# Kernel tuning notes

Hardware: AMD Instinct MI355X
Metric: run time of the kernel (lower is better)

## Reference

```python
import jax, jax.numpy as jnp
import numpy as np

WS = (4, 4, 4)      # window size (d, h, w)
SS = (2, 2, 2)      # shift size
HEADS = 4
EPS = 1e-6          # flax LayerNorm default epsilon


def _rel_pos_index(ws):
    # replicates the source exactly (np.meshgrid default 'xy' indexing)
    coords = np.stack(np.meshgrid(np.arange(ws[0]), np.arange(ws[1]), np.arange(ws[2])))
    cf = coords.reshape(3, -1)
    rc = (cf[:, :, None] - cf[:, None, :]).transpose(1, 2, 0).astype(np.int64)
    rc[:, :, 0] += ws[0] - 1
    rc[:, :, 1] += ws[1] - 1
    rc[:, :, 2] += ws[2] - 1
    rc[:, :, 0] *= (2 * ws[1] - 1) * (2 * ws[2] - 1)
    rc[:, :, 1] *= 2 * ws[2] - 1
    return rc.sum(-1)  # (n, n)


def _compute_mask(dp, hp, wp, ws, ss):
    # standard shifted-window attention mask: (nw, n, n) with 0 / -100
    img = np.zeros((1, dp, hp, wp, 1), np.float32)
    cnt = 0
    sls = lambda w, s: (slice(0, -w), slice(-w, -s), slice(-s, None))
    for d in sls(ws[0], ss[0]):
        for h in sls(ws[1], ss[1]):
            for w in sls(ws[2], ss[2]):
                img[:, d, h, w, :] = cnt
                cnt += 1
    mw = img.reshape(1, dp // ws[0], ws[0], hp // ws[1], ws[1], wp // ws[2], ws[2], 1)
    mw = mw.transpose(0, 1, 3, 5, 2, 4, 6, 7).reshape(-1, ws[0] * ws[1] * ws[2])
    am = mw[:, None, :] - mw[:, :, None]
    return np.where(am != 0, np.float32(-100.0), np.float32(0.0))


def window_partition(x, ws):
    b, d, h, w, c = x.shape
    x = x.reshape(b, d // ws[0], ws[0], h // ws[1], ws[1], w // ws[2], ws[2], c)
    return x.transpose(0, 1, 3, 5, 2, 4, 6, 7).reshape(-1, ws[0] * ws[1] * ws[2], c)


def window_reverse(windows, ws, dims):
    b, d, h, w = dims
    x = windows.reshape(b, d // ws[0], h // ws[1], w // ws[2], ws[0], ws[1], ws[2], -1)
    return x.transpose(0, 1, 4, 2, 5, 3, 6, 7).reshape(b, d, h, w, -1)


def layernorm(x, scale, bias):
    m = x.mean(-1, keepdims=True)
    v = x.var(-1, keepdims=True)
    return (x - m) * jax.lax.rsqrt(v + EPS) * scale + bias


def setup_inputs() -> dict:
    key = jax.random.key(0)
    ks = jax.random.split(key, 8)
    B, D, H, W, C = 2, 32, 64, 64, 128
    HID = 4 * C
    p = 0.02
    return {
        "x": jax.random.normal(ks[0], (B, D, H, W, C), jnp.float32),
        "mask": jnp.asarray(_compute_mask(D, H, W, WS, SS)),
        "norm1_scale": jnp.ones((C,), jnp.float32),
        "norm1_bias": jnp.zeros((C,), jnp.float32),
        "qkv_w": jax.random.normal(ks[1], (C, 3 * C), jnp.float32) * p,
        "rel_bias_table": jax.random.normal(ks[2], ((2 * WS[0] - 1) * (2 * WS[1] - 1) * (2 * WS[2] - 1), HEADS), jnp.float32) * p,
        "proj_w": jax.random.normal(ks[3], (C, C), jnp.float32) * p,
        "proj_b": jnp.zeros((C,), jnp.float32),
        "norm2_scale": jnp.ones((C,), jnp.float32),
        "norm2_bias": jnp.zeros((C,), jnp.float32),
        "mlp_w1": jax.random.normal(ks[4], (C, HID), jnp.float32) * p,
        "mlp_b1": jnp.zeros((HID,), jnp.float32),
        "mlp_w2": jax.random.normal(ks[5], (HID, C), jnp.float32) * p,
        "mlp_b2": jnp.zeros((C,), jnp.float32),
    }


def reference(x, mask, norm1_scale, norm1_bias, qkv_w, rel_bias_table, proj_w, proj_b,
              norm2_scale, norm2_bias, mlp_w1, mlp_b1, mlp_w2, mlp_b2):
    b, d, h, w, c = x.shape
    hd = c // HEADS
    scale = hd ** -0.5
    n = WS[0] * WS[1] * WS[2]

    shortcut = x
    xn = layernorm(x, norm1_scale, norm1_bias)
    # cyclic shift + window partition
    shifted = jnp.roll(xn, shift=(-SS[0], -SS[1], -SS[2]), axis=(1, 2, 3))
    xw = window_partition(shifted, WS)                      # (b*nw, n, c)
    bw = xw.shape[0]

    qkv = (xw @ qkv_w).reshape(bw, n, 3, HEADS, hd).transpose(2, 0, 3, 1, 4)
    q, k, v = qkv[0] * scale, qkv[1], qkv[2]                # (bw, heads, n, hd)
    attn = jnp.einsum('bhqd,bhkd->bhqk', q, k)              # (bw, heads, n, n)

    idx = _rel_pos_index(WS)
    bias = rel_bias_table[idx.reshape(-1)].reshape(n, n, HEADS).transpose(2, 0, 1)
    attn = attn + bias[None]

    nw = mask.shape[0]
    attn = attn.reshape(bw // nw, nw, HEADS, n, n) + mask[None, :, None]
    attn = jax.nn.softmax(attn.reshape(bw, HEADS, n, n), axis=-1)

    out = jnp.einsum('bhqk,bhkd->bhqd', attn, v)
    out = jnp.swapaxes(out, 1, 2).reshape(bw, n, c)
    out = out @ proj_w + proj_b

    attn_out = window_reverse(out, WS, (b, d, h, w))
    attn_out = jnp.roll(attn_out, shift=SS, axis=(1, 2, 3))

    x = shortcut + attn_out
    xn2 = layernorm(x, norm2_scale, norm2_bias)
    m = jax.nn.gelu(xn2 @ mlp_w1 + mlp_b1) @ mlp_w2 + mlp_b2
    return x + m
```

## Files before the change

kernel.cpp:

```cpp
#include <hip/hip_runtime.h>

typedef __bf16 bf16x8 __attribute__((ext_vector_type(8)));
typedef float f32x4 __attribute__((ext_vector_type(4)));
typedef unsigned short u16x4 __attribute__((ext_vector_type(4)));
typedef unsigned short u16x8 __attribute__((ext_vector_type(8)));

#define MFMA16(a,b,c) __builtin_amdgcn_mfma_f32_16x16x32_bf16((a),(b),(c),0,0,0)

__device__ __forceinline__ unsigned short f2bf(float f){
  return __builtin_bit_cast(unsigned short, static_cast<__bf16>(f));
}
__device__ __forceinline__ float bf2f(unsigned short h){
  unsigned u = ((unsigned)h)<<16;
  return __builtin_bit_cast(float, u);
}
__device__ __forceinline__ bf16x8 g_frag(const unsigned short* __restrict__ wf, int fragIdx, int lane){
  return __builtin_bit_cast(bf16x8, *reinterpret_cast<const u16x8*>(wf + (size_t)(fragIdx*64 + lane)*8));
}
__device__ __forceinline__ bf16x8 lds_frag(const unsigned short* base, int fragIdx, int lane){
  return __builtin_bit_cast(bf16x8, *reinterpret_cast<const u16x8*>(base + (fragIdx*64 + lane)*8));
}
__device__ __forceinline__ bf16x8 bc(u16x8 v){ return __builtin_bit_cast(bf16x8, v); }

__global__ void pack_w_kernel(const float* __restrict__ src, unsigned short* __restrict__ dst,
                              int MT, int KP, int M){
  int tid = blockIdx.x*256 + threadIdx.x;
  if (tid >= MT*KP*64) return;
  int lane = tid & 63;
  int t2 = tid >> 6;
  int kp = t2 % KP;
  int m = 16*(t2 / KP) + (lane & 15);
  int g = lane >> 4;
  u16x8 v;
#pragma unroll
  for (int j = 0; j < 8; ++j) {
    int k = 4*g + (j&3) + 16*(j>>2) + 32*kp;
    v[j] = f2bf(src[k*M + m]);
  }
  *reinterpret_cast<u16x8*>(&dst[(size_t)tid*8]) = v;
}

__global__ void prep_bias_kernel(const float* __restrict__ table, float* __restrict__ bias2){
  int o = blockIdx.x*256 + threadIdx.x;
  if (o >= 4*4*4*64*4) return;
  int r2 = o&3, lane = (o>>2)&63, nt = (o>>8)&3, mt = (o>>10)&3, h = o>>12;
  int g = lane>>4, l15 = lane&15;
  int key = 16*mt + 4*g + r2, q = 16*nt + l15;
  int da = ((q>>2)&3) - ((key>>2)&3) + 3;
  int ha = (q>>4)     - (key>>4)     + 3;
  int wa = (q&3)      - (key&3)      + 3;
  bias2[o] = table[((da*7+ha)*7+wa)*4 + h];
}

__global__ __launch_bounds__(256, 2)
void swin_block_kernel(const float* __restrict__ x,
                       const float* __restrict__ n1s, const float* __restrict__ n1b,
                       const unsigned short* __restrict__ wqk,
                       const unsigned short* __restrict__ wvb,
                       const float* __restrict__ bias2,
                       const unsigned short* __restrict__ wproj,
                       const float* __restrict__ projb,
                       const float* __restrict__ n2s, const float* __restrict__ n2b,
                       const unsigned short* __restrict__ w1f, const float* __restrict__ b1,
                       const unsigned short* __restrict__ w2f, const float* __restrict__ b2,
                       float* __restrict__ out)
{
  __shared__ __align__(16) unsigned short ldsA[16*64*8];
  __shared__ __align__(16) unsigned short ldsH[16*64*8];
  __shared__ int rid_s[64];

  const int tid  = threadIdx.x;
  const int lane = tid & 63;
  const int w    = tid >> 6;
  const int g    = lane >> 4;
  const int l15  = lane & 15;

  const int wb = blockIdx.x;
  const int b  = wb >> 11;
  const int r0 = wb & 2047;
  const int bd = r0 >> 8, bh = (r0 >> 4) & 15, bwi = r0 & 15;

  const int t = tid >> 2, qtr = tid & 3;
  const int wd = t >> 4, wh = (t >> 2) & 3, ww = t & 3;
  const int dco = (bd*4 + wd + 2) & 31;
  const int hco = (bh*4 + wh + 2) & 63;
  const int wco = (bwi*4 + ww + 2) & 63;
  const long tokl = ((long)((b*32 + dco)*64 + hco))*64 + wco;
  const float* xrow = x + tokl*128 + qtr*32;
  const int tileT = t >> 4, l15t = t & 15;

  u16x8 rsd[4];
  {
    float xr[32];
    float s = 0.f, sq = 0.f;
#pragma unroll
    for (int i = 0; i < 8; ++i) {
      float4 v = reinterpret_cast<const float4*>(xrow)[i];
      xr[4*i+0]=v.x; xr[4*i+1]=v.y; xr[4*i+2]=v.z; xr[4*i+3]=v.w;
      s  += v.x + v.y + v.z + v.w;
      sq += v.x*v.x + v.y*v.y + v.z*v.z + v.w*v.w;
    }
    s  += __shfl_xor(s, 1);  s  += __shfl_xor(s, 2);
    sq += __shfl_xor(sq, 1); sq += __shfl_xor(sq, 2);
    const float mean = s * 0.0078125f;
    const float rs   = rsqrtf(sq * 0.0078125f - mean*mean + 1e-6f);
#pragma unroll
    for (int i = 0; i < 8; ++i) {
      u16x4 o4;
#pragma unroll
      for (int j2 = 0; j2 < 4; ++j2) {
        int c = qtr*32 + 4*i + j2;
        o4[j2] = f2bf((xr[4*i+j2]-mean)*rs*n1s[c] + n1b[c]);
        rsd[i>>1][4*(i&1)+j2] = f2bf(xr[4*i+j2]);
      }
      *reinterpret_cast<u16x4*>(&ldsA[((tileT*4+qtr)*64 + l15t + 16*(i&3))*8 + 4*(i>>2)]) = o4;
    }
  }
  if (tid < 64) {
    int twd = tid >> 4, twh = (tid >> 2) & 3, tww = tid & 3;
    int rd = (bd == 7)  ? (twd < 2 ? 1 : 2) : 0;
    int rh = (bh == 15) ? (twh < 2 ? 1 : 2) : 0;
    int rw = (bwi == 15)? (tww < 2 ? 1 : 2) : 0;
    rid_s[tid] = rd*9 + rh*3 + rw;
  }
  __syncthreads();

  u16x8 Qf[4], Kf[4], Vf[2][2];
  {
    f32x4 acc[2][4];
#pragma unroll
    for (int mi=0;mi<2;++mi)
#pragma unroll
      for (int nt=0;nt<4;++nt){ f32x4 z={0.f,0.f,0.f,0.f}; acc[mi][nt]=z; }
#pragma unroll
    for (int kp=0;kp<4;++kp){
      bf16x8 bx[4];
#pragma unroll
      for (int nt=0;nt<4;++nt) bx[nt] = lds_frag(ldsA, nt*4+kp, lane);
#pragma unroll
      for (int mi=0;mi<2;++mi){
        bf16x8 a = g_frag(wqk, (2*w+mi)*4+kp, lane);
#pragma unroll
        for (int nt=0;nt<4;++nt) acc[mi][nt] = MFMA16(a, bx[nt], acc[mi][nt]);
      }
    }
#pragma unroll
    for (int nt=0;nt<4;++nt){
      u16x8 v;
#pragma unroll
      for (int j=0;j<8;++j) v[j] = f2bf(acc[j>>2][nt][j&3]*0.17677669529663687f);
      Qf[nt]=v;
    }
#pragma unroll
    for (int mi=0;mi<2;++mi)
#pragma unroll
      for (int nt=0;nt<4;++nt){ f32x4 z={0.f,0.f,0.f,0.f}; acc[mi][nt]=z; }
#pragma unroll
    for (int kp=0;kp<4;++kp){
      bf16x8 bx[4];
#pragma unroll
      for (int nt=0;nt<4;++nt) bx[nt] = lds_frag(ldsA, nt*4+kp, lane);
#pragma unroll
      for (int mi=0;mi<2;++mi){
        bf16x8 a = g_frag(wqk, (8+2*w+mi)*4+kp, lane);
#pragma unroll
        for (int nt=0;nt<4;++nt) acc[mi][nt] = MFMA16(a, bx[nt], acc[mi][nt]);
      }
    }
#pragma unroll
    for (int nt=0;nt<4;++nt){
      u16x8 v;
#pragma unroll
      for (int j=0;j<8;++j) v[j] = f2bf(acc[j>>2][nt][j&3]);
      Kf[nt]=v;
    }
    f32x4 vacc[4][2];
#pragma unroll
    for (int mt=0;mt<4;++mt)
#pragma unroll
      for (int c2=0;c2<2;++c2){ f32x4 z={0.f,0.f,0.f,0.f}; vacc[mt][c2]=z; }
#pragma unroll
    for (int kp=0;kp<4;++kp){
      bf16x8 ax[4];
#pragma unroll
      for (int mt=0;mt<4;++mt) ax[mt] = lds_frag(ldsA, mt*4+kp, lane);
#pragma unroll
      for (int c2=0;c2<2;++c2){
        bf16x8 bv = g_frag(wvb, (2*w+c2)*4+kp, lane);
#pragma unroll
        for (int mt=0;mt<4;++mt) vacc[mt][c2] = MFMA16(ax[mt], bv, vacc[mt][c2]);
      }
    }
#pragma unroll
    for (int c2=0;c2<2;++c2)
#pragma unroll
      for (int kpk=0;kpk<2;++kpk){
        u16x8 v;
#pragma unroll
        for (int j=0;j<8;++j) v[j] = f2bf(vacc[(j>>2)+2*kpk][c2][j&3]);
        Vf[c2][kpk]=v;
      }
  }
  __syncthreads();

  {
#pragma unroll
    for (int nt=0;nt<4;++nt){
      f32x4 sacc[4];
#pragma unroll
      for (int mt=0;mt<4;++mt){
        f32x4 z = {0.f,0.f,0.f,0.f};
        sacc[mt] = MFMA16(bc(Kf[mt]), bc(Qf[nt]), z);
      }
      const int ridq = rid_s[16*nt + l15];
#pragma unroll
      for (int mt=0;mt<4;++mt){
        int4 rk = *reinterpret_cast<const int4*>(&rid_s[16*mt + 4*g]);
        float4 bv = reinterpret_cast<const float4*>(bias2)[((w*4+mt)*4+nt)*64 + lane];
        sacc[mt][0] += bv.x + (rk.x != ridq ? -100.f : 0.f);
        sacc[mt][1] += bv.y + (rk.y != ridq ? -100.f : 0.f);
        sacc[mt][2] += bv.z + (rk.z != ridq ? -100.f : 0.f);
        sacc[mt][3] += bv.w + (rk.w != ridq ? -100.f : 0.f);
      }
      float mx = -1e30f;
#pragma unroll
      for (int mt=0;mt<4;++mt)
#pragma unroll
        for (int r2=0;r2<4;++r2) mx = fmaxf(mx, sacc[mt][r2]);
      mx = fmaxf(mx, __shfl_xor(mx, 16));
      mx = fmaxf(mx, __shfl_xor(mx, 32));
      float sum = 0.f;
#pragma unroll
      for (int mt=0;mt<4;++mt)
#pragma unroll
        for (int r2=0;r2<4;++r2){
          float p = __expf(sacc[mt][r2] - mx);
          sacc[mt][r2] = p; sum += p;
        }
      sum += __shfl_xor(sum, 16);
      sum += __shfl_xor(sum, 32);
      const float inv = 1.f / sum;
      u16x8 Pf0, Pf1;
#pragma unroll
      for (int j=0;j<8;++j){
        Pf0[j] = f2bf(sacc[(j>>2)  ][j&3]*inv);
        Pf1[j] = f2bf(sacc[(j>>2)+2][j&3]*inv);
      }
      f32x4 oa[2];
#pragma unroll
      for (int c2=0;c2<2;++c2){
        f32x4 z = {0.f,0.f,0.f,0.f};
        z = MFMA16(bc(Vf[c2][0]), bc(Pf0), z);
        oa[c2] = MFMA16(bc(Vf[c2][1]), bc(Pf1), z);
      }
      u16x8 v;
#pragma unroll
      for (int j=0;j<8;++j) v[j] = f2bf(oa[j>>2][j&3]);
      *reinterpret_cast<u16x8*>(&ldsA[((nt*4+w)*64+lane)*8]) = v;
    }
  }
  __syncthreads();

  {
    f32x4 pacc[2][4];
#pragma unroll
    for (int mi=0;mi<2;++mi)
#pragma unroll
      for (int nt=0;nt<4;++nt){ f32x4 z={0.f,0.f,0.f,0.f}; pacc[mi][nt]=z; }
#pragma unroll
    for (int kp=0;kp<4;++kp){
      bf16x8 bo[4];
#pragma unroll
      for (int nt=0;nt<4;++nt) bo[nt] = lds_frag(ldsA, nt*4+kp, lane);
#pragma unroll
      for (int mi=0;mi<2;++mi){
        bf16x8 a = g_frag(wproj, (2*w+mi)*4+kp, lane);
#pragma unroll
        for (int nt=0;nt<4;++nt) pacc[mi][nt] = MFMA16(a, bo[nt], pacc[mi][nt]);
      }
    }
#pragma unroll
    for (int mi=0;mi<2;++mi)
#pragma unroll
      for (int r2=0;r2<4;++r2){
        const float pb = projb[16*(2*w+mi) + 4*g + r2];
#pragma unroll
        for (int nt=0;nt<4;++nt) pacc[mi][nt][r2] += pb;
      }
    __syncthreads();
#pragma unroll
    for (int nt=0;nt<4;++nt){
      u16x8 v;
#pragma unroll
      for (int j=0;j<8;++j) v[j] = f2bf(pacc[j>>2][nt][j&3]);
      *reinterpret_cast<u16x8*>(&ldsA[((nt*4+w)*64+lane)*8]) = v;
    }
  }
  __syncthreads();

  {
    float xv[32];
    float s2 = 0.f, sq2 = 0.f;
#pragma unroll
    for (int i = 0; i < 8; ++i) {
      u16x4 sg = *reinterpret_cast<const u16x4*>(&ldsA[((tileT*4+qtr)*64 + l15t + 16*(i&3))*8 + 4*(i>>2)]);
#pragma unroll
      for (int j2 = 0; j2 < 4; ++j2) {
        float v2 = bf2f(rsd[i>>1][4*(i&1)+j2]) + bf2f(sg[j2]);
        xv[4*i+j2] = v2;
        s2 += v2; sq2 += v2*v2;
      }
    }
    s2  += __shfl_xor(s2, 1);  s2  += __shfl_xor(s2, 2);
    sq2 += __shfl_xor(sq2, 1); sq2 += __shfl_xor(sq2, 2);
    const float mean2 = s2*0.0078125f;
    const float rs2 = rsqrtf(sq2*0.0078125f - mean2*mean2 + 1e-6f);
#pragma unroll
    for (int i = 0; i < 8; ++i) {
      u16x4 o4;
#pragma unroll
      for (int j2 = 0; j2 < 4; ++j2) {
        int c = qtr*32 + 4*i + j2;
        o4[j2] = f2bf((xv[4*i+j2]-mean2)*rs2*n2s[c] + n2b[c]);
        rsd[i>>1][4*(i&1)+j2] = f2bf(xv[4*i+j2]);
      }
      *reinterpret_cast<u16x4*>(&ldsA[((tileT*4+qtr)*64 + l15t + 16*(i&3))*8 + 4*(i>>2)]) = o4;
    }
  }
  __syncthreads();

  {
    f32x4 macc[2][4];
#pragma unroll
    for (int mi=0;mi<2;++mi)
#pragma unroll
      for (int nt=0;nt<4;++nt){ f32x4 z={0.f,0.f,0.f,0.f}; macc[mi][nt]=z; }
#pragma unroll
    for (int cc=0;cc<4;++cc){
      f32x4 hacc[2][4];
#pragma unroll
      for (int mi=0;mi<2;++mi)
#pragma unroll
        for (int nt=0;nt<4;++nt){ f32x4 z={0.f,0.f,0.f,0.f}; hacc[mi][nt]=z; }
#pragma unroll
      for (int kp=0;kp<4;++kp){
        bf16x8 bn[4];
#pragma unroll
        for (int nt=0;nt<4;++nt) bn[nt] = lds_frag(ldsA, nt*4+kp, lane);
#pragma unroll
        for (int mi=0;mi<2;++mi){
          bf16x8 a = g_frag(w1f, (cc*8+2*w+mi)*4+kp, lane);
#pragma unroll
          for (int nt=0;nt<4;++nt) hacc[mi][nt] = MFMA16(a, bn[nt], hacc[mi][nt]);
        }
      }
#pragma unroll
      for (int nt=0;nt<4;++nt){
        u16x8 hv;
#pragma unroll
        for (int j=0;j<8;++j){
          const int mi = j>>2, r2 = j&3;
          const int hch = cc*128 + 32*w + 16*mi + 4*g + r2;
          float v2 = hacc[mi][nt][r2] + b1[hch];
          float gg = 0.7978845608028654f*(v2 + 0.044715f*v2*v2*v2);
          float ge = v2 / (1.f + __expf(-2.f*gg));
          hv[j] = f2bf(ge);
        }
        *reinterpret_cast<u16x8*>(&ldsH[((nt*4+w)*64+lane)*8]) = hv;
      }
      __syncthreads();
#pragma unroll
      for (int kph=0;kph<4;++kph){
        bf16x8 bhf[4];
#pragma unroll
        for (int nt=0;nt<4;++nt) bhf[nt] = lds_frag(ldsH, nt*4+kph, lane);
#pragma unroll
        for (int mi=0;mi<2;++mi){
          bf16x8 a2 = g_frag(w2f, (2*w+mi)*16 + cc*4 + kph, lane);
#pragma unroll
          for (int nt=0;nt<4;++nt) macc[mi][nt] = MFMA16(a2, bhf[nt], macc[mi][nt]);
        }
      }
      __syncthreads();
    }
#pragma unroll
    for (int nt=0;nt<4;++nt){
      u16x8 v;
#pragma unroll
      for (int j=0;j<8;++j){
        const int mi = j>>2, r2 = j&3;
        v[j] = f2bf(macc[mi][nt][r2] + b2[16*(2*w+mi) + 4*g + r2]);
      }
      *reinterpret_cast<u16x8*>(&ldsA[((nt*4+w)*64+lane)*8]) = v;
    }
  }
  __syncthreads();

  {
    float* orow = out + tokl*128 + qtr*32;
#pragma unroll
    for (int i = 0; i < 8; ++i) {
      u16x4 mv = *reinterpret_cast<const u16x4*>(&ldsA[((tileT*4+qtr)*64 + l15t + 16*(i&3))*8 + 4*(i>>2)]);
      float4 v;
      v.x = bf2f(rsd[i>>1][4*(i&1)+0]) + bf2f(mv[0]);
      v.y = bf2f(rsd[i>>1][4*(i&1)+1]) + bf2f(mv[1]);
      v.z = bf2f(rsd[i>>1][4*(i&1)+2]) + bf2f(mv[2]);
      v.w = bf2f(rsd[i>>1][4*(i&1)+3]) + bf2f(mv[3]);
      reinterpret_cast<float4*>(orow)[i] = v;
    }
  }
}

extern "C" void kernel_launch(void* const* d_in, const int* in_sizes, int n_in,
                              void* d_out, int out_size, void* d_ws, size_t ws_size,
                              hipStream_t stream) {
  (void)in_sizes; (void)n_in; (void)out_size; (void)ws_size;
  const float* x    = (const float*)d_in[0];
  const float* n1s  = (const float*)d_in[2];
  const float* n1b  = (const float*)d_in[3];
  const float* qkvw = (const float*)d_in[4];
  const float* tbl  = (const float*)d_in[5];
  const float* pw   = (const float*)d_in[6];
  const float* pb   = (const float*)d_in[7];
  const float* n2s  = (const float*)d_in[8];
  const float* n2b  = (const float*)d_in[9];
  const float* w1   = (const float*)d_in[10];
  const float* b1   = (const float*)d_in[11];
  const float* w2   = (const float*)d_in[12];
  const float* b2   = (const float*)d_in[13];
  float* out = (float*)d_out;

  unsigned short* wqk_f   = (unsigned short*)d_ws;
  unsigned short* wvb_f   = wqk_f   + 16*4*64*8;
  unsigned short* wproj_f = wvb_f   + 8*4*64*8;
  unsigned short* w1_f    = wproj_f + 8*4*64*8;
  unsigned short* w2_f    = w1_f    + 32*4*64*8;
  float*          bias2   = (float*)(w2_f + 8*16*64*8);

  pack_w_kernel<<<16, 256, 0, stream>>>(qkvw,       wqk_f,  16, 4, 384);
  pack_w_kernel<<< 8, 256, 0, stream>>>(qkvw + 256, wvb_f,   8, 4, 384);
  pack_w_kernel<<< 8, 256, 0, stream>>>(pw,   wproj_f, 8, 4, 128);
  pack_w_kernel<<<32, 256, 0, stream>>>(w1,   w1_f,   32, 4, 512);
  pack_w_kernel<<<32, 256, 0, stream>>>(w2,   w2_f,    8,16, 128);
  prep_bias_kernel<<<64, 256, 0, stream>>>(tbl, bias2);

  swin_block_kernel<<<4096, 256, 0, stream>>>(x, n1s, n1b, wqk_f, wvb_f, bias2, wproj_f, pb,
                                              n2s, n2b, w1_f, b1, w2_f, b2, out);
}
```

Baseline: 496.2 us.

## Restructure proj/MLP to per-wave token tiles, fuse QKV loops and prep kernels

The projection and MLP stages are reorganized so each wave owns one 16-token tile and computes all output channels. The MLP hidden activations then stay in registers and feed the second GEMM directly, which removes the per-chunk LDS round trip and the block barriers. The Q, K and V projections share a single loop over LDS fragments. The shift mask is skipped for interior windows, and the six prep launches are merged into one kernel. In exchange, each wave now loads the full weight matrices from global memory, and the kernel carries more accumulator registers.

```diff
diff --git a/kernel.cpp b/kernel.cpp
--- a/kernel.cpp
+++ b/kernel.cpp
@@ -22,9 +22,9 @@
 }
 __device__ __forceinline__ bf16x8 bc(u16x8 v){ return __builtin_bit_cast(bf16x8, v); }
 
-__global__ void pack_w_kernel(const float* __restrict__ src, unsigned short* __restrict__ dst,
-                              int MT, int KP, int M){
-  int tid = blockIdx.x*256 + threadIdx.x;
+__device__ __forceinline__ void pack_body(const float* __restrict__ src, unsigned short* __restrict__ dst,
+                                          int blk, int MT, int KP, int M){
+  int tid = blk*256 + threadIdx.x;
   if (tid >= MT*KP*64) return;
   int lane = tid & 63;
   int t2 = tid >> 6;
@@ -40,16 +40,27 @@
   *reinterpret_cast<u16x8*>(&dst[(size_t)tid*8]) = v;
 }
 
-__global__ void prep_bias_kernel(const float* __restrict__ table, float* __restrict__ bias2){
-  int o = blockIdx.x*256 + threadIdx.x;
-  if (o >= 4*4*4*64*4) return;
+__global__ void prep_kernel(const float* __restrict__ qkvw, const float* __restrict__ pw,
+                            const float* __restrict__ w1, const float* __restrict__ w2,
+                            const float* __restrict__ tbl,
+                            unsigned short* __restrict__ wqk_f, unsigned short* __restrict__ wvb_f,
+                            unsigned short* __restrict__ wproj_f,
+                            unsigned short* __restrict__ w1_f, unsigned short* __restrict__ w2_f,
+                            float* __restrict__ bias2){
+  const int bb = blockIdx.x;
+  if (bb < 16)      { pack_body(qkvw,       wqk_f,   bb,      16, 4, 384); return; }
+  else if (bb < 24) { pack_body(qkvw + 256, wvb_f,   bb-16,    8, 4, 384); return; }
+  else if (bb < 32) { pack_body(pw,         wproj_f, bb-24,    8, 4, 128); return; }
+  else if (bb < 64) { pack_body(w1,         w1_f,    bb-32,   32, 4, 512); return; }
+  else if (bb < 96) { pack_body(w2,         w2_f,    bb-64,    8,16, 128); return; }
+  const int o = (bb-96)*256 + threadIdx.x;
   int r2 = o&3, lane = (o>>2)&63, nt = (o>>8)&3, mt = (o>>10)&3, h = o>>12;
   int g = lane>>4, l15 = lane&15;
   int key = 16*mt + 4*g + r2, q = 16*nt + l15;
   int da = ((q>>2)&3) - ((key>>2)&3) + 3;
   int ha = (q>>4)     - (key>>4)     + 3;
   int wa = (q&3)      - (key&3)      + 3;
-  bias2[o] = table[((da*7+ha)*7+wa)*4 + h];
+  bias2[o] = tbl[((da*7+ha)*7+wa)*4 + h];
 }
 
 __global__ __launch_bounds__(256, 2)
@@ -79,6 +90,7 @@
   const int b  = wb >> 11;
   const int r0 = wb & 2047;
   const int bd = r0 >> 8, bh = (r0 >> 4) & 15, bwi = r0 & 15;
+  const bool edge = (bd==7) || (bh==15) || (bwi==15);
 
   const int t = tid >> 2, qtr = tid & 3;
   const int wd = t >> 4, wh = (t >> 2) & 3, ww = t & 3;
@@ -116,7 +128,7 @@
       *reinterpret_cast<u16x4*>(&ldsA[((tileT*4+qtr)*64 + l15t + 16*(i&3))*8 + 4*(i>>2)]) = o4;
     }
   }
-  if (tid < 64) {
+  if (edge && tid < 64) {
     int twd = tid >> 4, twh = (tid >> 2) & 3, tww = tid & 3;
     int rd = (bd == 7)  ? (twd < 2 ? 1 : 2) : 0;
     int rh = (bh == 15) ? (twh < 2 ? 1 : 2) : 0;
@@ -127,69 +139,44 @@
 
   u16x8 Qf[4], Kf[4], Vf[2][2];
   {
-    f32x4 acc[2][4];
-#pragma unroll
-    for (int mi=0;mi<2;++mi)
-#pragma unroll
-      for (int nt=0;nt<4;++nt){ f32x4 z={0.f,0.f,0.f,0.f}; acc[mi][nt]=z; }
+    f32x4 qacc[2][4], kacc[2][4], vacc[4][2];
+#pragma unroll
+    for (int a2=0;a2<2;++a2)
+#pragma unroll
+      for (int b4=0;b4<4;++b4){ f32x4 z={0.f,0.f,0.f,0.f}; qacc[a2][b4]=z; kacc[a2][b4]=z; vacc[b4][a2]=z; }
 #pragma unroll
     for (int kp=0;kp<4;++kp){
-      bf16x8 bx[4];
-#pragma unroll
-      for (int nt=0;nt<4;++nt) bx[nt] = lds_frag(ldsA, nt*4+kp, lane);
+      bf16x8 fx[4];
+#pragma unroll
+      for (int nt=0;nt<4;++nt) fx[nt] = lds_frag(ldsA, nt*4+kp, lane);
 #pragma unroll
       for (int mi=0;mi<2;++mi){
-        bf16x8 a = g_frag(wqk, (2*w+mi)*4+kp, lane);
-#pragma unroll
-        for (int nt=0;nt<4;++nt) acc[mi][nt] = MFMA16(a, bx[nt], acc[mi][nt]);
-      }
-    }
-#pragma unroll
-    for (int nt=0;nt<4;++nt){
-      u16x8 v;
-#pragma unroll
-      for (int j=0;j<8;++j) v[j] = f2bf(acc[j>>2][nt][j&3]*0.17677669529663687f);
-      Qf[nt]=v;
-    }
-#pragma unroll
-    for (int mi=0;mi<2;++mi)
-#pragma unroll
-      for (int nt=0;nt<4;++nt){ f32x4 z={0.f,0.f,0.f,0.f}; acc[mi][nt]=z; }
-#pragma unroll
-    for (int kp=0;kp<4;++kp){
-      bf16x8 bx[4];
-#pragma unroll
-      for (int nt=0;nt<4;++nt) bx[nt] = lds_frag(ldsA, nt*4+kp, lane);
+        bf16x8 aq = g_frag(wqk, (2*w+mi)*4+kp, lane);
+#pragma unroll
+        for (int nt=0;nt<4;++nt) qacc[mi][nt] = MFMA16(aq, fx[nt], qacc[mi][nt]);
+      }
 #pragma unroll
       for (int mi=0;mi<2;++mi){
-        bf16x8 a = g_frag(wqk, (8+2*w+mi)*4+kp, lane);
-#pragma unroll
-        for (int nt=0;nt<4;++nt) acc[mi][nt] = MFMA16(a, bx[nt], acc[mi][nt]);
-      }
-    }
-#pragma unroll
-    for (int nt=0;nt<4;++nt){
-      u16x8 v;
-#pragma unroll
-      for (int j=0;j<8;++j) v[j] = f2bf(acc[j>>2][nt][j&3]);
-      Kf[nt]=v;
-    }
-    f32x4 vacc[4][2];
-#pragma unroll
-    for (int mt=0;mt<4;++mt)
-#pragma unroll
-      for (int c2=0;c2<2;++c2){ f32x4 z={0.f,0.f,0.f,0.f}; vacc[mt][c2]=z; }
-#pragma unroll
-    for (int kp=0;kp<4;++kp){
-      bf16x8 ax[4];
-#pragma unroll
-      for (int mt=0;mt<4;++mt) ax[mt] = lds_frag(ldsA, mt*4+kp, lane);
+        bf16x8 ak = g_frag(wqk, (8+2*w+mi)*4+kp, lane);
+#pragma unroll
+        for (int nt=0;nt<4;++nt) kacc[mi][nt] = MFMA16(ak, fx[nt], kacc[mi][nt]);
+      }
 #pragma unroll
       for (int c2=0;c2<2;++c2){
         bf16x8 bv = g_frag(wvb, (2*w+c2)*4+kp, lane);
 #pragma unroll
-        for (int mt=0;mt<4;++mt) vacc[mt][c2] = MFMA16(ax[mt], bv, vacc[mt][c2]);
-      }
+        for (int mt=0;mt<4;++mt) vacc[mt][c2] = MFMA16(fx[mt], bv, vacc[mt][c2]);
+      }
+    }
+#pragma unroll
+    for (int nt=0;nt<4;++nt){
+      u16x8 vq, vk;
+#pragma unroll
+      for (int j=0;j<8;++j){
+        vq[j] = f2bf(qacc[j>>2][nt][j&3]*0.17677669529663687f);
+        vk[j] = f2bf(kacc[j>>2][nt][j&3]);
+      }
+      Qf[nt]=vq; Kf[nt]=vk;
     }
 #pragma unroll
     for (int c2=0;c2<2;++c2)
@@ -204,6 +191,11 @@
   __syncthreads();
 
   {
+    int4 rk[4];
+    if (edge){
+#pragma unroll
+      for (int mt=0;mt<4;++mt) rk[mt] = *reinterpret_cast<const int4*>(&rid_s[16*mt + 4*g]);
+    }
 #pragma unroll
     for (int nt=0;nt<4;++nt){
       f32x4 sacc[4];
@@ -212,15 +204,22 @@
         f32x4 z = {0.f,0.f,0.f,0.f};
         sacc[mt] = MFMA16(bc(Kf[mt]), bc(Qf[nt]), z);
       }
-      const int ridq = rid_s[16*nt + l15];
-#pragma unroll
-      for (int mt=0;mt<4;++mt){
-        int4 rk = *reinterpret_cast<const int4*>(&rid_s[16*mt + 4*g]);
-        float4 bv = reinterpret_cast<const float4*>(bias2)[((w*4+mt)*4+nt)*64 + lane];
-        sacc[mt][0] += bv.x + (rk.x != ridq ? -100.f : 0.f);
-        sacc[mt][1] += bv.y + (rk.y != ridq ? -100.f : 0.f);
-        sacc[mt][2] += bv.z + (rk.z != ridq ? -100.f : 0.f);
-        sacc[mt][3] += bv.w + (rk.w != ridq ? -100.f : 0.f);
+      if (edge){
+        const int ridq = rid_s[16*nt + l15];
+#pragma unroll
+        for (int mt=0;mt<4;++mt){
+          float4 bv = reinterpret_cast<const float4*>(bias2)[((w*4+mt)*4+nt)*64 + lane];
+          sacc[mt][0] += bv.x + (rk[mt].x != ridq ? -100.f : 0.f);
+          sacc[mt][1] += bv.y + (rk[mt].y != ridq ? -100.f : 0.f);
+          sacc[mt][2] += bv.z + (rk[mt].z != ridq ? -100.f : 0.f);
+          sacc[mt][3] += bv.w + (rk[mt].w != ridq ? -100.f : 0.f);
+        }
+      } else {
+#pragma unroll
+        for (int mt=0;mt<4;++mt){
+          float4 bv = reinterpret_cast<const float4*>(bias2)[((w*4+mt)*4+nt)*64 + lane];
+          sacc[mt][0] += bv.x; sacc[mt][1] += bv.y; sacc[mt][2] += bv.z; sacc[mt][3] += bv.w;
+        }
       }
       float mx = -1e30f;
 #pragma unroll
@@ -262,38 +261,27 @@
   __syncthreads();
 
   {
-    f32x4 pacc[2][4];
-#pragma unroll
-    for (int mi=0;mi<2;++mi)
-#pragma unroll
-      for (int nt=0;nt<4;++nt){ f32x4 z={0.f,0.f,0.f,0.f}; pacc[mi][nt]=z; }
+    f32x4 pacc[8];
+#pragma unroll
+    for (int mt=0;mt<8;++mt){ f32x4 z={0.f,0.f,0.f,0.f}; pacc[mt]=z; }
 #pragma unroll
     for (int kp=0;kp<4;++kp){
-      bf16x8 bo[4];
-#pragma unroll
-      for (int nt=0;nt<4;++nt) bo[nt] = lds_frag(ldsA, nt*4+kp, lane);
-#pragma unroll
-      for (int mi=0;mi<2;++mi){
-        bf16x8 a = g_frag(wproj, (2*w+mi)*4+kp, lane);
-#pragma unroll
-        for (int nt=0;nt<4;++nt) pacc[mi][nt] = MFMA16(a, bo[nt], pacc[mi][nt]);
-      }
-    }
-#pragma unroll
-    for (int mi=0;mi<2;++mi)
-#pragma unroll
-      for (int r2=0;r2<4;++r2){
-        const float pb = projb[16*(2*w+mi) + 4*g + r2];
-#pragma unroll
-        for (int nt=0;nt<4;++nt) pacc[mi][nt][r2] += pb;
-      }
-    __syncthreads();
-#pragma unroll
-    for (int nt=0;nt<4;++nt){
+      bf16x8 bo = lds_frag(ldsA, w*4+kp, lane);
+#pragma unroll
+      for (int mt=0;mt<8;++mt)
+        pacc[mt] = MFMA16(g_frag(wproj, mt*4+kp, lane), bo, pacc[mt]);
+    }
+#pragma unroll
+    for (int mt=0;mt<8;++mt){
+      float4 pb = *reinterpret_cast<const float4*>(&projb[16*mt + 4*g]);
+      pacc[mt][0]+=pb.x; pacc[mt][1]+=pb.y; pacc[mt][2]+=pb.z; pacc[mt][3]+=pb.w;
+    }
+#pragma unroll
+    for (int q2=0;q2<4;++q2){
       u16x8 v;
 #pragma unroll
-      for (int j=0;j<8;++j) v[j] = f2bf(pacc[j>>2][nt][j&3]);
-      *reinterpret_cast<u16x8*>(&ldsA[((nt*4+w)*64+lane)*8]) = v;
+      for (int j=0;j<8;++j) v[j] = f2bf(pacc[2*q2+(j>>2)][j&3]);
+      *reinterpret_cast<u16x8*>(&ldsH[((w*4+q2)*64+lane)*8]) = v;
     }
   }
   __syncthreads();
@@ -303,7 +291,7 @@
     float s2 = 0.f, sq2 = 0.f;
 #pragma unroll
     for (int i = 0; i < 8; ++i) {
-      u16x4 sg = *reinterpret_cast<const u16x4*>(&ldsA[((tileT*4+qtr)*64 + l15t + 16*(i&3))*8 + 4*(i>>2)]);
+      u16x4 sg = *reinterpret_cast<const u16x4*>(&ldsH[((tileT*4+qtr)*64 + l15t + 16*(i&3))*8 + 4*(i>>2)]);
 #pragma unroll
       for (int j2 = 0; j2 < 4; ++j2) {
         float v2 = bf2f(rsd[i>>1][4*(i&1)+j2]) + bf2f(sg[j2]);
@@ -330,68 +318,48 @@
   __syncthreads();
 
   {
-    f32x4 macc[2][4];
-#pragma unroll
-    for (int mi=0;mi<2;++mi)
-#pragma unroll
-      for (int nt=0;nt<4;++nt){ f32x4 z={0.f,0.f,0.f,0.f}; macc[mi][nt]=z; }
-#pragma unroll
-    for (int cc=0;cc<4;++cc){
-      f32x4 hacc[2][4];
-#pragma unroll
-      for (int mi=0;mi<2;++mi)
-#pragma unroll
-        for (int nt=0;nt<4;++nt){ f32x4 z={0.f,0.f,0.f,0.f}; hacc[mi][nt]=z; }
-#pragma unroll
-      for (int kp=0;kp<4;++kp){
-        bf16x8 bn[4];
-#pragma unroll
-        for (int nt=0;nt<4;++nt) bn[nt] = lds_frag(ldsA, nt*4+kp, lane);
-#pragma unroll
-        for (int mi=0;mi<2;++mi){
-          bf16x8 a = g_frag(w1f, (cc*8+2*w+mi)*4+kp, lane);
-#pragma unroll
-          for (int nt=0;nt<4;++nt) hacc[mi][nt] = MFMA16(a, bn[nt], hacc[mi][nt]);
-        }
-      }
-#pragma unroll
-      for (int nt=0;nt<4;++nt){
-        u16x8 hv;
-#pragma unroll
-        for (int j=0;j<8;++j){
-          const int mi = j>>2, r2 = j&3;
-          const int hch = cc*128 + 32*w + 16*mi + 4*g + r2;
-          float v2 = hacc[mi][nt][r2] + b1[hch];
+    bf16x8 Bn[4];
+#pragma unroll
+    for (int kp=0;kp<4;++kp) Bn[kp] = lds_frag(ldsA, w*4+kp, lane);
+    f32x4 macc[8];
+#pragma unroll
+    for (int mt=0;mt<8;++mt){ f32x4 z={0.f,0.f,0.f,0.f}; macc[mt]=z; }
+#pragma unroll 4
+    for (int kp2=0;kp2<16;++kp2){
+      f32x4 hacc[2];
+#pragma unroll
+      for (int hi=0;hi<2;++hi){
+        f32x4 z = {0.f,0.f,0.f,0.f};
+#pragma unroll
+        for (int kp1=0;kp1<4;++kp1)
+          z = MFMA16(g_frag(w1f, (2*kp2+hi)*4+kp1, lane), Bn[kp1], z);
+        hacc[hi] = z;
+      }
+      u16x8 bhv;
+#pragma unroll
+      for (int hi=0;hi<2;++hi){
+        float4 bb = *reinterpret_cast<const float4*>(&b1[32*kp2 + 16*hi + 4*g]);
+#pragma unroll
+        for (int r2=0;r2<4;++r2){
+          float v2 = hacc[hi][r2] + (&bb.x)[r2];
           float gg = 0.7978845608028654f*(v2 + 0.044715f*v2*v2*v2);
           float ge = v2 / (1.f + __expf(-2.f*gg));
-          hv[j] = f2bf(ge);
+          bhv[4*hi+r2] = f2bf(ge);
         }
-        *reinterpret_cast<u16x8*>(&ldsH[((nt*4+w)*64+lane)*8]) = hv;
-      }
-      __syncthreads();
-#pragma unroll
-      for (int kph=0;kph<4;++kph){
-        bf16x8 bhf[4];
-#pragma unroll
-        for (int nt=0;nt<4;++nt) bhf[nt] = lds_frag(ldsH, nt*4+kph, lane);
-#pragma unroll
-        for (int mi=0;mi<2;++mi){
-          bf16x8 a2 = g_frag(w2f, (2*w+mi)*16 + cc*4 + kph, lane);
-#pragma unroll
-          for (int nt=0;nt<4;++nt) macc[mi][nt] = MFMA16(a2, bhf[nt], macc[mi][nt]);
-        }
-      }
-      __syncthreads();
-    }
-#pragma unroll
-    for (int nt=0;nt<4;++nt){
+      }
+#pragma unroll
+      for (int mt=0;mt<8;++mt)
+        macc[mt] = MFMA16(g_frag(w2f, mt*16+kp2, lane), bc(bhv), macc[mt]);
+    }
+#pragma unroll
+    for (int q2=0;q2<4;++q2){
       u16x8 v;
 #pragma unroll
       for (int j=0;j<8;++j){
-        const int mi = j>>2, r2 = j&3;
-        v[j] = f2bf(macc[mi][nt][r2] + b2[16*(2*w+mi) + 4*g + r2]);
-      }
-      *reinterpret_cast<u16x8*>(&ldsA[((nt*4+w)*64+lane)*8]) = v;
+        const int mt = 2*q2+(j>>2);
+        v[j] = f2bf(macc[mt][j&3] + b2[16*mt + 4*g + (j&3)]);
+      }
+      *reinterpret_cast<u16x8*>(&ldsH[((w*4+q2)*64+lane)*8]) = v;
     }
   }
   __syncthreads();
@@ -400,7 +368,7 @@
     float* orow = out + tokl*128 + qtr*32;
 #pragma unroll
     for (int i = 0; i < 8; ++i) {
-      u16x4 mv = *reinterpret_cast<const u16x4*>(&ldsA[((tileT*4+qtr)*64 + l15t + 16*(i&3))*8 + 4*(i>>2)]);
+      u16x4 mv = *reinterpret_cast<const u16x4*>(&ldsH[((tileT*4+qtr)*64 + l15t + 16*(i&3))*8 + 4*(i>>2)]);
       float4 v;
       v.x = bf2f(rsd[i>>1][4*(i&1)+0]) + bf2f(mv[0]);
       v.y = bf2f(rsd[i>>1][4*(i&1)+1]) + bf2f(mv[1]);
@@ -437,12 +405,8 @@
   unsigned short* w2_f    = w1_f    + 32*4*64*8;
   float*          bias2   = (float*)(w2_f + 8*16*64*8);
 
-  pack_w_kernel<<<16, 256, 0, stream>>>(qkvw,       wqk_f,  16, 4, 384);
-  pack_w_kernel<<< 8, 256, 0, stream>>>(qkvw + 256, wvb_f,   8, 4, 384);
-  pack_w_kernel<<< 8, 256, 0, stream>>>(pw,   wproj_f, 8, 4, 128);
-  pack_w_kernel<<<32, 256, 0, stream>>>(w1,   w1_f,   32, 4, 512);
-  pack_w_kernel<<<32, 256, 0, stream>>>(w2,   w2_f,    8,16, 128);
-  prep_bias_kernel<<<64, 256, 0, stream>>>(tbl, bias2);
+  prep_kernel<<<160, 256, 0, stream>>>(qkvw, pw, w1, w2, tbl,
+                                       wqk_f, wvb_f, wproj_f, w1_f, w2_f, bias2);
 
   swin_block_kernel<<<4096, 256, 0, stream>>>(x, n1s, n1b, wqk_f, wvb_f, bias2, wproj_f, pb,
                                               n2s, n2b, w1_f, b1, w2_f, b2, out);
```

After: 866.7 us. 74.7% more time.
